# Kernel tuning notes

Measured on AMD Instinct MI355X. Metric: run time of the kernel, lower is better.

The kernel has to match this reference:

```python
import jax, jax.numpy as jnp
import numpy as np

B, T, SEQ = 8, 129, 128
H, N, NL, NE, V = 512, 64, 4, 128, 18

def _gelu(x):
    return jax.nn.gelu(x, approximate=False)

def _conv2d(x, w, b, stride):
    y = jax.lax.conv_general_dilated(x, w, (stride, stride), 'VALID',
                                     dimension_numbers=('NCHW', 'OIHW', 'NCHW'))
    return y + b[None, :, None, None]

def _layernorm(x, g, b, eps=1e-5):
    mu = jnp.mean(x, axis=-1, keepdims=True)
    var = jnp.mean(jnp.square(x - mu), axis=-1, keepdims=True)
    return (x - mu) * jax.lax.rsqrt(var + eps) * g + b

def _s4_kernel(log_dt, A_re, A_im, C_re, C_im, L):
    # Diagonal SSM (ZOH discretization, B=1): K[h,l] = 2*Re(sum_n Ceff * exp(dt*A)^l)
    dt = jnp.exp(log_dt)[:, None]                  # [H,1]
    A = A_re + 1j * A_im                            # [H,N] complex64
    dtA = (dt * A).astype(jnp.complex64)
    C = (C_re + 1j * C_im).astype(jnp.complex64)
    Ceff = C * (jnp.exp(dtA) - 1.0) / A             # [H,N]
    vand = jnp.exp(dtA[:, :, None] * jnp.arange(L, dtype=jnp.float32))  # [H,N,L]
    return 2.0 * jnp.einsum('hn,hnl->hl', Ceff, vand).real

def _fft_conv(u, K, D):
    # u: [B,H,L]  K: [H,L]  causal conv via zero-padded FFT
    L = u.shape[-1]
    n = 2 * L
    Uf = jnp.fft.rfft(u, n=n)
    Kf = jnp.fft.rfft(K, n=n)
    y = jnp.fft.irfft(Uf * Kf[None], n=n)[..., :L]
    return y + D[None, :, None] * u

def setup_inputs() -> dict:
    key = jax.random.key(0)
    ks = jax.random.split(key, 32)
    d = {}
    d['states'] = jax.random.uniform(ks[0], (B, T, 4, 84, 84), dtype=jnp.float32)
    d['actions'] = jax.random.randint(ks[1], (B, T), 0, V)
    d['rtgs'] = jax.random.uniform(ks[2], (B, T, 1), dtype=jnp.float32)
    s = 0.02
    d['enc_w1'] = jax.random.normal(ks[3], (32, 4, 8, 8)) * s
    d['enc_b1'] = jnp.zeros((32,))
    d['enc_w2'] = jax.random.normal(ks[4], (64, 32, 4, 4)) * s
    d['enc_b2'] = jnp.zeros((64,))
    d['enc_w3'] = jax.random.normal(ks[5], (64, 64, 3, 3)) * s
    d['enc_b3'] = jnp.zeros((64,))
    d['enc_lw'] = jax.random.normal(ks[6], (3136, NE)) * s
    d['enc_lb'] = jnp.zeros((NE,))
    d['ret_w'] = jax.random.normal(ks[7], (1, NE)) * s
    d['ret_b'] = jnp.zeros((NE,))
    d['act_emb'] = jax.random.normal(ks[8], (V, NE)) * s
    d['proj_w'] = jax.random.normal(ks[9], (3 * NE, H)) * s
    d['proj_b'] = jnp.zeros((H,))
    d['pre_w'] = jax.random.normal(ks[10], (H, H)) * s
    d['pre_b'] = jnp.zeros((H,))
    d['ln_g'] = jnp.ones((NL, H))
    d['ln_b'] = jnp.zeros((NL, H))
    lo, hi = np.log(1e-3), np.log(1e-1)
    d['log_dt'] = lo + jax.random.uniform(ks[11], (NL, H)) * (hi - lo)
    d['A_re'] = -0.5 * jnp.ones((NL, H, N))
    d['A_im'] = jnp.broadcast_to(np.pi * jnp.arange(N, dtype=jnp.float32), (NL, H, N)).copy()
    d['C_re'] = jax.random.normal(ks[12], (NL, H, N)) * (0.5 ** 0.5)
    d['C_im'] = jax.random.normal(ks[13], (NL, H, N)) * (0.5 ** 0.5)
    d['Dp'] = jax.random.normal(ks[14], (NL, H))
    d['aft_w'] = jax.random.normal(ks[15], (NL, H, H)) * s
    d['aft_b'] = jnp.zeros((NL, H))
    d['out_w'] = jax.random.normal(ks[16], (H, V)) * s
    return d

def reference(states, actions, rtgs, enc_w1, enc_b1, enc_w2, enc_b2, enc_w3, enc_b3,
              enc_lw, enc_lb, ret_w, ret_b, act_emb, proj_w, proj_b, pre_w, pre_b,
              ln_g, ln_b, log_dt, A_re, A_im, C_re, C_im, Dp, aft_w, aft_b, out_w):
    S = actions.shape[1] - 1  # del_r = 1
    # state encoder over B*S frames
    x = states[:, 1:].reshape(-1, 4, 84, 84)
    x = jax.nn.relu(_conv2d(x, enc_w1, enc_b1, 4))
    x = jax.nn.relu(_conv2d(x, enc_w2, enc_b2, 2))
    x = jax.nn.relu(_conv2d(x, enc_w3, enc_b3, 1))
    se = jnp.tanh(x.reshape(x.shape[0], -1) @ enc_lw + enc_lb)          # [B*S, NE]
    ae = jnp.tanh(act_emb[actions[:, :S].reshape(-1)])                   # [B*S, NE]
    re = jnp.tanh(rtgs[:, :S].reshape(-1, 1) @ ret_w + ret_b)            # [B*S, NE]
    u = jnp.concatenate([se, ae, re], axis=-1) @ proj_w + proj_b
    u = u.reshape(states.shape[0], S, H)
    y = _gelu(u) @ pre_w + pre_b                                          # beforeblock
    for i in range(NL):
        r = _layernorm(y, ln_g[i], ln_b[i])
        v = jnp.transpose(r, (0, 2, 1))                                   # [B,H,S]
        K = _s4_kernel(log_dt[i], A_re[i], A_im[i], C_re[i], C_im[i], S)
        c = _fft_conv(v, K, Dp[i])
        c = jnp.transpose(c, (0, 2, 1))                                   # [B,S,H]
        c = _gelu(_gelu(c) @ aft_w[i] + aft_b[i])
        y = c + y                                                          # s4_resnet
    logits = y @ out_w                                                     # [B,S,V]
    return logits
```

## Files before the change

kernel.cpp:

```cpp
#include <hip/hip_runtime.h>

#define Bq 8
#define Tq 129
#define Sq 128
#define Hq 512
#define Nq 64
#define NLq 4
#define NEq 128
#define Vq 18

typedef unsigned short u16;
typedef unsigned int u32;
typedef __attribute__((ext_vector_type(8))) short short8v;
typedef __attribute__((ext_vector_type(4))) float f32x4;

__device__ __forceinline__ float gelu_f(float x) {
  return 0.5f * x * (1.0f + erff(x * 0.70710678118654752f));
}

__device__ __forceinline__ u16 f2b(float x) {
  union { float f; unsigned int u; } v; v.f = x;
  unsigned int r = v.u + 0x7FFFu + ((v.u >> 16) & 1u);
  return (u16)(r >> 16);
}

__device__ __forceinline__ float b2f_lo(u32 u) {
  union { unsigned int u; float f; } v; v.u = u << 16; return v.f;
}
__device__ __forceinline__ float b2f_hi(u32 u) {
  union { unsigned int u; float f; } v; v.u = u & 0xffff0000u; return v.f;
}

__global__ __launch_bounds__(256) void wprep_k(const float* __restrict__ w1,
    const float* __restrict__ w2, const float* __restrict__ w3,
    u16* __restrict__ B1t, u16* __restrict__ B2t, u16* __restrict__ B3t) {
  int i = blockIdx.x * 256 + threadIdx.x;
  if (i < 8192) {
    int n = i >> 8, k = i & 255;
    int ic = k >> 6, ky = (k >> 3) & 7, kx = k & 7;
    B1t[i] = f2b(w1[((n * 4 + ic) * 8 + ky) * 8 + kx]);
  } else if (i < 8192 + 32768) {
    int j = i - 8192;
    int n = j >> 9, k = j & 511;
    int kyx = k >> 5, ic = k & 31, ky = kyx >> 2, kx = kyx & 3;
    B2t[j] = f2b(w2[((n * 32 + ic) * 4 + ky) * 4 + kx]);
  } else if (i < 8192 + 32768 + 36864) {
    int j = i - 40960;
    int n = j / 576, k = j - n * 576;
    int ic = k & 63, kyx = k >> 6, ky = kyx / 3, kx = kyx % 3;
    B3t[j] = f2b(w3[((n * 64 + ic) * 3 + ky) * 3 + kx]);
  }
}

__global__ __launch_bounds__(256) void wtrans_k(const float* __restrict__ enc_lw,
    const float* __restrict__ proj_w, const float* __restrict__ pre_w,
    const float* __restrict__ aft_w, const float* __restrict__ out_w,
    u16* __restrict__ Wt_enc, u16* __restrict__ Wt_proj, u16* __restrict__ Wt_pre,
    u16* __restrict__ Wt_aft, u16* __restrict__ Wt_out) {
  __shared__ u16 T[64][65];
  int bid = blockIdx.x;
  const float* src; u16* dst; int K, N, kt, nt, t;
  if (bid < 98)       { t = bid;       src = enc_lw; dst = Wt_enc;  K = 3136; N = 128; kt = t >> 1; nt = t & 1; }
  else if (bid < 146) { t = bid - 98;  src = proj_w; dst = Wt_proj; K = 384;  N = 512; kt = t >> 3; nt = t & 7; }
  else if (bid < 210) { t = bid - 146; src = pre_w;  dst = Wt_pre;  K = 512;  N = 512; kt = t >> 3; nt = t & 7; }
  else if (bid < 466) { t = bid - 210; int L = t >> 6; t &= 63;
                        src = aft_w + (size_t)L * 262144; dst = Wt_aft + (size_t)L * 262144;
                        K = 512; N = 512; kt = t >> 3; nt = t & 7; }
  else                { t = bid - 466; src = out_w;  dst = Wt_out;  K = 512;  N = 18;  kt = t;      nt = 0; }
  int k0 = kt * 64, n0 = nt * 64;
  #pragma unroll
  for (int it = 0; it < 16; it++) {
    int idx = it * 256 + threadIdx.x;
    int rr = idx >> 6, cc = idx & 63;
    float v = (n0 + cc < N) ? src[(size_t)(k0 + rr) * N + n0 + cc] : 0.f;
    T[cc][rr] = f2b(v);
  }
  __syncthreads();
  #pragma unroll
  for (int it = 0; it < 16; it++) {
    int idx = it * 256 + threadIdx.x;
    int rr = idx >> 6, cc = idx & 63;
    dst[(size_t)(n0 + rr) * K + k0 + cc] = T[rr][cc];
  }
}

template<bool AF32, int EPI>
__global__ __launch_bounds__(256) void mgemm(const void* __restrict__ Av,
    const u16* __restrict__ Wt, const float* __restrict__ bias,
    const float* __restrict__ res, void* __restrict__ Cv,
    int M, int K, int N, int ldc) {
  __shared__ u16 As[64][40];
  __shared__ u16 Bs[64][40];
  int tid = threadIdx.x;
  int bn = blockIdx.x * 64, bm = blockIdx.y * 64;
  int lane = tid & 63, w = tid >> 6;
  int q = lane >> 4, r = lane & 15;
  int wm = (w >> 1) * 32, wn = (w & 1) * 32;
  int am = tid >> 2, ak = (tid & 3) * 8;
  f32x4 acc[2][2] = {};
  for (int k0 = 0; k0 < K; k0 += 32) {
    if constexpr (AF32) {
      const float* A = (const float*)Av;
      const float* src = A + (size_t)(bm + am) * K + k0 + ak;
      float4 v0 = *(const float4*)src;
      float4 v1 = *(const float4*)(src + 4);
      ushort4 lo, hi;
      lo.x = f2b(v0.x); lo.y = f2b(v0.y); lo.z = f2b(v0.z); lo.w = f2b(v0.w);
      hi.x = f2b(v1.x); hi.y = f2b(v1.y); hi.z = f2b(v1.z); hi.w = f2b(v1.w);
      *(ushort4*)&As[am][ak] = lo;
      *(ushort4*)&As[am][ak + 4] = hi;
    } else {
      const u16* A = (const u16*)Av;
      *(short8v*)&As[am][ak] = *(const short8v*)(A + (size_t)(bm + am) * K + k0 + ak);
    }
    *(short8v*)&Bs[am][ak] = *(const short8v*)(Wt + (size_t)(bn + am) * K + k0 + ak);
    __syncthreads();
    short8v a0 = *(const short8v*)&As[wm + r][q * 8];
    short8v a1 = *(const short8v*)&As[wm + 16 + r][q * 8];
    short8v b0 = *(const short8v*)&Bs[wn + r][q * 8];
    short8v b1 = *(const short8v*)&Bs[wn + 16 + r][q * 8];
    acc[0][0] = __builtin_amdgcn_mfma_f32_16x16x32_bf16(a0, b0, acc[0][0], 0, 0, 0);
    acc[0][1] = __builtin_amdgcn_mfma_f32_16x16x32_bf16(a0, b1, acc[0][1], 0, 0, 0);
    acc[1][0] = __builtin_amdgcn_mfma_f32_16x16x32_bf16(a1, b0, acc[1][0], 0, 0, 0);
    acc[1][1] = __builtin_amdgcn_mfma_f32_16x16x32_bf16(a1, b1, acc[1][1], 0, 0, 0);
    __syncthreads();
  }
  #pragma unroll
  for (int ms = 0; ms < 2; ms++) {
    #pragma unroll
    for (int ns = 0; ns < 2; ns++) {
      #pragma unroll
      for (int reg = 0; reg < 4; reg++) {
        int m = bm + wm + ms * 16 + q * 4 + reg;
        int n = bn + wn + ns * 16 + r;
        if (n < N) {
          float v = acc[ms][ns][reg] + (bias ? bias[n] : 0.f);
          if (EPI == 0) ((float*)Cv)[(size_t)m * ldc + n] = v;
          if (EPI == 2) ((u16*)Cv)[(size_t)m * ldc + n] = f2b(gelu_f(v));
          if (EPI == 3) ((float*)Cv)[(size_t)m * ldc + n] = gelu_f(v) + res[(size_t)m * ldc + n];
        }
      }
    }
  }
}

__global__ __launch_bounds__(256) void enc_gemm(const u16* __restrict__ A,
    const u16* __restrict__ Wt, float* __restrict__ Cp) {
  __shared__ u16 As[64][40];
  __shared__ u16 Bs[64][40];
  int tid = threadIdx.x;
  int bn = blockIdx.x * 64, bm = blockIdx.y * 64, kc = blockIdx.z;
  int lane = tid & 63, w = tid >> 6;
  int q = lane >> 4, r = lane & 15;
  int wm = (w >> 1) * 32, wn = (w & 1) * 32;
  int am = tid >> 2, ak = (tid & 3) * 8;
  f32x4 acc[2][2] = {};
  int kend = kc * 448 + 448;
  for (int k0 = kc * 448; k0 < kend; k0 += 32) {
    *(short8v*)&As[am][ak] = *(const short8v*)(A + (size_t)(bm + am) * 3136 + k0 + ak);
    *(short8v*)&Bs[am][ak] = *(const short8v*)(Wt + (size_t)(bn + am) * 3136 + k0 + ak);
    __syncthreads();
    short8v a0 = *(const short8v*)&As[wm + r][q * 8];
    short8v a1 = *(const short8v*)&As[wm + 16 + r][q * 8];
    short8v b0 = *(const short8v*)&Bs[wn + r][q * 8];
    short8v b1 = *(const short8v*)&Bs[wn + 16 + r][q * 8];
    acc[0][0] = __builtin_amdgcn_mfma_f32_16x16x32_bf16(a0, b0, acc[0][0], 0, 0, 0);
    acc[0][1] = __builtin_amdgcn_mfma_f32_16x16x32_bf16(a0, b1, acc[0][1], 0, 0, 0);
    acc[1][0] = __builtin_amdgcn_mfma_f32_16x16x32_bf16(a1, b0, acc[1][0], 0, 0, 0);
    acc[1][1] = __builtin_amdgcn_mfma_f32_16x16x32_bf16(a1, b1, acc[1][1], 0, 0, 0);
    __syncthreads();
  }
  #pragma unroll
  for (int ms = 0; ms < 2; ms++)
    #pragma unroll
    for (int ns = 0; ns < 2; ns++)
      #pragma unroll
      for (int reg = 0; reg < 4; reg++) {
        int m = bm + wm + ms * 16 + q * 4 + reg;
        int n = bn + wn + ns * 16 + r;
        Cp[(size_t)(kc * 1024 + m) * 128 + n] = acc[ms][ns][reg];
      }
}

__global__ __launch_bounds__(256) void enc_red(const float* __restrict__ Cp,
    const float* __restrict__ bias, u16* __restrict__ uin) {
  int idx = blockIdx.x * 256 + threadIdx.x;
  int m = idx >> 7, n = idx & 127;
  float s = bias[n];
  #pragma unroll
  for (int kc = 0; kc < 7; kc++) s += Cp[(size_t)(kc * 1024 + m) * 128 + n];
  uin[(size_t)m * 384 + n] = f2b(tanhf(s));
}

__global__ __launch_bounds__(256) void conv1_mfma(const float* __restrict__ states,
    const u16* __restrict__ B1t, const float* __restrict__ bias, u16* __restrict__ out) {
  __shared__ u16 lds[28224];
  int fr = blockIdx.x;
  int b = fr >> 7, s = fr & 127;
  const float* in = states + (size_t)(b * Tq + s + 1) * 28224;
  int tid = threadIdx.x;
  #pragma unroll
  for (int it = 0; it < 28; it++) {
    int idx = tid + it * 256;
    if (idx < 7056) {
      float4 v = ((const float4*)in)[idx];
      ushort4 uv;
      uv.x = f2b(v.x); uv.y = f2b(v.y); uv.z = f2b(v.z); uv.w = f2b(v.w);
      *(ushort4*)&lds[idx * 4] = uv;
    }
  }
  int lane = tid & 63, w = tid >> 6;
  int q = lane >> 4, r = lane & 15;
  short8v bfr[2][8];
  #pragma unroll
  for (int nt = 0; nt < 2; nt++)
    #pragma unroll
    for (int ks = 0; ks < 8; ks++)
      bfr[nt][ks] = *(const short8v*)(B1t + (nt * 16 + r) * 256 + ks * 32 + q * 8);
  __syncthreads();
  for (int mt = w; mt < 25; mt += 4) {
    int m = mt * 16 + r;
    int oy = m / 20, ox = m % 20;
    f32x4 acc0 = {0.f, 0.f, 0.f, 0.f}, acc1 = {0.f, 0.f, 0.f, 0.f};
    #pragma unroll
    for (int ks = 0; ks < 8; ks++) {
      int k0 = ks * 32 + q * 8;
      int ic = k0 >> 6, ky = (k0 >> 3) & 7;
      int ai = ic * 7056 + (oy * 4 + ky) * 84 + ox * 4;
      ushort4 lo = *(const ushort4*)&lds[ai];
      ushort4 hi = *(const ushort4*)&lds[ai + 4];
      short8v av;
      av[0] = (short)lo.x; av[1] = (short)lo.y; av[2] = (short)lo.z; av[3] = (short)lo.w;
      av[4] = (short)hi.x; av[5] = (short)hi.y; av[6] = (short)hi.z; av[7] = (short)hi.w;
      acc0 = __builtin_amdgcn_mfma_f32_16x16x32_bf16(av, bfr[0][ks], acc0, 0, 0, 0);
      acc1 = __builtin_amdgcn_mfma_f32_16x16x32_bf16(av, bfr[1][ks], acc1, 0, 0, 0);
    }
    #pragma unroll
    for (int reg = 0; reg < 4; reg++) {
      int pos = mt * 16 + q * 4 + reg;
      out[(size_t)fr * 12800 + pos * 32 + r]      = f2b(fmaxf(acc0[reg] + bias[r], 0.f));
      out[(size_t)fr * 12800 + pos * 32 + 16 + r] = f2b(fmaxf(acc1[reg] + bias[16 + r], 0.f));
    }
  }
}

__global__ __launch_bounds__(256) void conv2_mfma(const u16* __restrict__ in_,
    const u16* __restrict__ B2t, const float* __restrict__ bias, u16* __restrict__ out) {
  __shared__ u16 lds[12800];
  int fr = blockIdx.x;
  int tid = threadIdx.x;
  const short8v* src = (const short8v*)(in_ + (size_t)fr * 12800);
  short8v* dst = (short8v*)lds;
  #pragma unroll
  for (int it = 0; it < 7; it++) {
    int idx = tid + it * 256;
    if (idx < 1600) dst[idx] = src[idx];
  }
  int lane = tid & 63, w = tid >> 6;
  int q = lane >> 4, r = lane & 15;
  int n = w * 16 + r;
  short8v bfr[16];
  #pragma unroll
  for (int ks = 0; ks < 16; ks++)
    bfr[ks] = *(const short8v*)(B2t + n * 512 + ks * 32 + q * 8);
  __syncthreads();
  float bn = bias[n];
  #pragma unroll
  for (int mt = 0; mt < 6; mt++) {
    int m = mt * 16 + r; if (m > 80) m = 80;
    int oy = m / 9, ox = m % 9;
    f32x4 acc = {0.f, 0.f, 0.f, 0.f};
    #pragma unroll
    for (int ks = 0; ks < 16; ks++) {
      int ky = ks >> 2, kx = ks & 3;
      int ai = ((oy * 2 + ky) * 20 + ox * 2 + kx) * 32 + q * 8;
      short8v av = *(const short8v*)&lds[ai];
      acc = __builtin_amdgcn_mfma_f32_16x16x32_bf16(av, bfr[ks], acc, 0, 0, 0);
    }
    #pragma unroll
    for (int reg = 0; reg < 4; reg++) {
      int pos = mt * 16 + q * 4 + reg;
      if (pos < 81)
        out[(size_t)fr * 5184 + pos * 64 + n] = f2b(fmaxf(acc[reg] + bn, 0.f));
    }
  }
}

__global__ __launch_bounds__(256) void conv3_mfma(const u16* __restrict__ in_,
    const u16* __restrict__ B3t, const float* __restrict__ bias, u16* __restrict__ out) {
  __shared__ u16 lds[5184];
  int fr = blockIdx.x;
  int tid = threadIdx.x;
  const short8v* src = (const short8v*)(in_ + (size_t)fr * 5184);
  short8v* dst = (short8v*)lds;
  #pragma unroll
  for (int it = 0; it < 3; it++) {
    int idx = tid + it * 256;
    if (idx < 648) dst[idx] = src[idx];
  }
  int lane = tid & 63, w = tid >> 6;
  int q = lane >> 4, r = lane & 15;
  int n = w * 16 + r;
  short8v bfr[18];
  #pragma unroll
  for (int ks = 0; ks < 18; ks++)
    bfr[ks] = *(const short8v*)(B3t + n * 576 + ks * 32 + q * 8);
  __syncthreads();
  float bn = bias[n];
  #pragma unroll
  for (int mt = 0; mt < 4; mt++) {
    int m = mt * 16 + r; if (m > 48) m = 48;
    int oy = m / 7, ox = m % 7;
    f32x4 acc = {0.f, 0.f, 0.f, 0.f};
    #pragma unroll
    for (int ks = 0; ks < 18; ks++) {
      int kyx = ks >> 1;
      int ky = kyx / 3, kx = kyx % 3;
      int ic0 = (ks & 1) * 32 + q * 8;
      int ai = ((oy + ky) * 9 + ox + kx) * 64 + ic0;
      short8v av = *(const short8v*)&lds[ai];
      acc = __builtin_amdgcn_mfma_f32_16x16x32_bf16(av, bfr[ks], acc, 0, 0, 0);
    }
    #pragma unroll
    for (int reg = 0; reg < 4; reg++) {
      int pos = mt * 16 + q * 4 + reg;
      if (pos < 49)
        out[(size_t)fr * 3136 + n * 49 + pos] = f2b(fmaxf(acc[reg] + bn, 0.f));
    }
  }
}

__global__ __launch_bounds__(256) void embed_k(const int* __restrict__ actions,
    const float* __restrict__ rtgs, const float* __restrict__ act_emb,
    const float* __restrict__ ret_w, const float* __restrict__ ret_b,
    u16* __restrict__ uin) {
  int f = blockIdx.x;
  int b = f >> 7, s = f & 127;
  int e = threadIdx.x;
  if (e < 128) {
    int a = actions[b * Tq + s];
    uin[(size_t)f * 384 + 128 + e] = f2b(tanhf(act_emb[a * NEq + e]));
  } else {
    int ee = e - 128;
    uin[(size_t)f * 384 + 256 + ee] =
        f2b(tanhf(fmaf(rtgs[b * Tq + s], ret_w[ee], ret_b[ee])));
  }
}

__global__ __launch_bounds__(64) void s4k_gen(const float* __restrict__ log_dt,
    const float* __restrict__ A_re, const float* __restrict__ A_im,
    const float* __restrict__ C_re, const float* __restrict__ C_im,
    u16* __restrict__ Ktb) {
  __shared__ float con[64][129];
  int lh = blockIdx.x;
  int n = threadIdx.x;
  float dt = expf(log_dt[lh]);
  float ar = A_re[(size_t)lh * Nq + n], ai = A_im[(size_t)lh * Nq + n];
  float al = dt * ar, be = dt * ai;
  float er = expf(al);
  float wr = er * cosf(be), wi = er * sinf(be);
  float zr = wr - 1.0f, zi = wi;
  float den = 1.0f / (ar * ar + ai * ai);
  float tr = (zr * ar + zi * ai) * den, ti = (zi * ar - zr * ai) * den;
  float Cr = C_re[(size_t)lh * Nq + n], Ci = C_im[(size_t)lh * Nq + n];
  float cr = Cr * tr - Ci * ti, ci = Cr * ti + Ci * tr;
  float curr = 1.0f, curi = 0.0f;
  for (int l = 0; l < Sq; l++) {
    con[n][l] = cr * curr - ci * curi;
    float nr = curr * wr - curi * wi;
    curi = curr * wi + curi * wr;
    curr = nr;
  }
  __syncthreads();
  int layer = lh >> 9, h = lh & 511;
  #pragma unroll
  for (int li = n; li < Sq; li += 64) {
    float s = 0.f;
    for (int j = 0; j < 64; j++) s += con[j][li];
    Ktb[((size_t)layer * Sq + li) * Hq + h] = f2b(2.0f * s);
  }
}

__global__ __launch_bounds__(256) void ln_k(const float* __restrict__ y,
    const float* __restrict__ g, const float* __restrict__ b, u16* __restrict__ r) {
  int row = blockIdx.x * 4 + (threadIdx.x >> 6);
  int lane = threadIdx.x & 63;
  const float* x = y + (size_t)row * Hq;
  float v[8], s = 0.f, s2 = 0.f;
  #pragma unroll
  for (int j = 0; j < 8; j++) {
    v[j] = x[lane + j * 64];
    s += v[j];
    s2 += v[j] * v[j];
  }
  #pragma unroll
  for (int o = 32; o >= 1; o >>= 1) {
    s += __shfl_xor(s, o);
    s2 += __shfl_xor(s2, o);
  }
  float mu = s * (1.f / Hq);
  float var = s2 * (1.f / Hq) - mu * mu;
  float inv = rsqrtf(var + 1e-5f);
  u16* out = r + (size_t)row * Hq;
  #pragma unroll
  for (int j = 0; j < 8; j++) {
    int h = lane + j * 64;
    out[h] = f2b((v[j] - mu) * inv * g[h] + b[h]);
  }
}

__global__ __launch_bounds__(256) void sconv_k(const u16* __restrict__ r,
    const u16* __restrict__ Kt, const float* __restrict__ D, u16* __restrict__ cact) {
  int s = blockIdx.x, b = blockIdx.y;
  int t = threadIdx.x;
  const u32* rb = (const u32*)(r + (size_t)b * Sq * Hq) + t;
  const u32* kp = (const u32*)Kt + t;
  float2 d = ((const float2*)D)[t];
  u32 rs = rb[(size_t)s * 256];
  float acc0 = d.x * b2f_lo(rs), acc1 = d.y * b2f_hi(rs);
  int j = 0;
  for (; j + 4 <= s + 1; j += 4) {
    u32 k0 = kp[(size_t)(j + 0) * 256];
    u32 k1 = kp[(size_t)(j + 1) * 256];
    u32 k2 = kp[(size_t)(j + 2) * 256];
    u32 k3 = kp[(size_t)(j + 3) * 256];
    u32 r0 = rb[(size_t)(s - j - 0) * 256];
    u32 r1 = rb[(size_t)(s - j - 1) * 256];
    u32 r2 = rb[(size_t)(s - j - 2) * 256];
    u32 r3 = rb[(size_t)(s - j - 3) * 256];
    acc0 = fmaf(b2f_lo(k0), b2f_lo(r0), acc0); acc1 = fmaf(b2f_hi(k0), b2f_hi(r0), acc1);
    acc0 = fmaf(b2f_lo(k1), b2f_lo(r1), acc0); acc1 = fmaf(b2f_hi(k1), b2f_hi(r1), acc1);
    acc0 = fmaf(b2f_lo(k2), b2f_lo(r2), acc0); acc1 = fmaf(b2f_hi(k2), b2f_hi(r2), acc1);
    acc0 = fmaf(b2f_lo(k3), b2f_lo(r3), acc0); acc1 = fmaf(b2f_hi(k3), b2f_hi(r3), acc1);
  }
  for (; j <= s; j++) {
    u32 kv = kp[(size_t)j * 256];
    u32 rv = rb[(size_t)(s - j) * 256];
    acc0 = fmaf(b2f_lo(kv), b2f_lo(rv), acc0);
    acc1 = fmaf(b2f_hi(kv), b2f_hi(rv), acc1);
  }
  u32 outv = (u32)f2b(gelu_f(acc0)) | ((u32)f2b(gelu_f(acc1)) << 16);
  ((u32*)(cact + ((size_t)b * Sq + s) * Hq))[t] = outv;
}

extern "C" void kernel_launch(void* const* d_in, const int* in_sizes, int n_in,
                              void* d_out, int out_size, void* d_ws, size_t ws_size,
                              hipStream_t stream) {
  const float* states  = (const float*)d_in[0];
  const int*   actions = (const int*)  d_in[1];
  const float* rtgs    = (const float*)d_in[2];
  const float* enc_w1  = (const float*)d_in[3];
  const float* enc_b1  = (const float*)d_in[4];
  const float* enc_w2  = (const float*)d_in[5];
  const float* enc_b2  = (const float*)d_in[6];
  const float* enc_w3  = (const float*)d_in[7];
  const float* enc_b3  = (const float*)d_in[8];
  const float* enc_lw  = (const float*)d_in[9];
  const float* enc_lb  = (const float*)d_in[10];
  const float* ret_w   = (const float*)d_in[11];
  const float* ret_b   = (const float*)d_in[12];
  const float* act_emb = (const float*)d_in[13];
  const float* proj_w  = (const float*)d_in[14];
  const float* proj_b  = (const float*)d_in[15];
  const float* pre_w   = (const float*)d_in[16];
  const float* pre_b   = (const float*)d_in[17];
  const float* ln_g    = (const float*)d_in[18];
  const float* ln_b    = (const float*)d_in[19];
  const float* log_dt  = (const float*)d_in[20];
  const float* A_re    = (const float*)d_in[21];
  const float* A_im    = (const float*)d_in[22];
  const float* C_re    = (const float*)d_in[23];
  const float* C_im    = (const float*)d_in[24];
  const float* Dp      = (const float*)d_in[25];
  const float* aft_w   = (const float*)d_in[26];
  const float* aft_b   = (const float*)d_in[27];
  const float* out_w   = (const float*)d_in[28];

  u16* Wt_enc  = (u16*)d_ws;
  u16* Wt_proj = Wt_enc + 401408;
  u16* Wt_pre  = Wt_proj + 196608;
  u16* Wt_aft  = Wt_pre + 262144;
  u16* Wt_out  = Wt_aft + 1048576;
  u16* B1t = Wt_out + 32768;
  u16* B2t = B1t + 8192;
  u16* B3t = B2t + 32768;
  u16* o1  = B3t + 36864;
  u16* o2  = o1 + 13107200;
  u16* x3b = o2 + 5308416;
  u16* uin = x3b + 3211264;
  u16* uact = uin + 393216;
  u16* cact = uact + 524288;
  u16* rb16 = cact + 524288;
  u16* Ktb  = rb16 + 524288;
  float* y  = (float*)(Ktb + 262144);
  float* Cp = y + 524288;

  wprep_k<<<304, 256, 0, stream>>>(enc_w1, enc_w2, enc_w3, B1t, B2t, B3t);
  wtrans_k<<<474, 256, 0, stream>>>(enc_lw, proj_w, pre_w, aft_w, out_w,
                                    Wt_enc, Wt_proj, Wt_pre, Wt_aft, Wt_out);
  conv1_mfma<<<1024, 256, 0, stream>>>(states, B1t, enc_b1, o1);
  conv2_mfma<<<1024, 256, 0, stream>>>(o1, B2t, enc_b2, o2);
  conv3_mfma<<<1024, 256, 0, stream>>>(o2, B3t, enc_b3, x3b);
  enc_gemm<<<dim3(2, 16, 7), 256, 0, stream>>>(x3b, Wt_enc, Cp);
  enc_red<<<512, 256, 0, stream>>>(Cp, enc_lb, uin);
  embed_k<<<1024, 256, 0, stream>>>(actions, rtgs, act_emb, ret_w, ret_b, uin);
  mgemm<false, 2><<<dim3(8, 16), 256, 0, stream>>>(uin, Wt_proj, proj_b, nullptr, uact,
                                                   1024, 384, 512, 512);
  mgemm<false, 0><<<dim3(8, 16), 256, 0, stream>>>(uact, Wt_pre, pre_b, nullptr, y,
                                                   1024, 512, 512, 512);
  s4k_gen<<<2048, 64, 0, stream>>>(log_dt, A_re, A_im, C_re, C_im, Ktb);

  for (int i = 0; i < NLq; i++) {
    ln_k<<<256, 256, 0, stream>>>(y, ln_g + i * Hq, ln_b + i * Hq, rb16);
    sconv_k<<<dim3(128, 8), 256, 0, stream>>>(rb16, Ktb + (size_t)i * Sq * Hq,
                                              Dp + i * Hq, cact);
    mgemm<false, 3><<<dim3(8, 16), 256, 0, stream>>>(cact, Wt_aft + (size_t)i * Hq * Hq,
                                                     aft_b + i * Hq, y, y,
                                                     1024, 512, 512, 512);
  }
  mgemm<true, 0><<<dim3(1, 16), 256, 0, stream>>>(y, Wt_out, nullptr, nullptr,
                                                  (float*)d_out, 1024, 512, Vq, Vq);
}
```

Measured before the change: 268.0 us.

## Merge prep kernels, fuse embed/reduce, tile causal conv in LDS, deepen GEMM K-stage

Merges the two weight-prep kernels into one launch and the encoder reduction with the embedding kernel. The layernorm apply step moves into a new LDS-tiled causal convolution that reuses kernel and input values across 8 outputs per thread, in place of strided global loads per output. The generic GEMM now stages 128 K elements per barrier pair, and conv1 runs with 512 threads. The aim is fewer launches, fewer barriers and less global traffic, at the cost of more LDS and registers and only 128 blocks for the conv kernel.

After: 225.8 us. 15.8% less time.

```diff
diff --git a/kernel.cpp b/kernel.cpp
--- a/kernel.cpp
+++ b/kernel.cpp
@@ -31,34 +31,36 @@
   union { unsigned int u; float f; } v; v.u = u & 0xffff0000u; return v.f;
 }
 
-__global__ __launch_bounds__(256) void wprep_k(const float* __restrict__ w1,
-    const float* __restrict__ w2, const float* __restrict__ w3,
+__global__ __launch_bounds__(256) void prep_k(
+    const float* __restrict__ enc_lw, const float* __restrict__ proj_w,
+    const float* __restrict__ pre_w, const float* __restrict__ aft_w,
+    const float* __restrict__ out_w,
+    const float* __restrict__ w1, const float* __restrict__ w2,
+    const float* __restrict__ w3,
+    u16* __restrict__ Wt_enc, u16* __restrict__ Wt_proj, u16* __restrict__ Wt_pre,
+    u16* __restrict__ Wt_aft, u16* __restrict__ Wt_out,
     u16* __restrict__ B1t, u16* __restrict__ B2t, u16* __restrict__ B3t) {
-  int i = blockIdx.x * 256 + threadIdx.x;
-  if (i < 8192) {
-    int n = i >> 8, k = i & 255;
-    int ic = k >> 6, ky = (k >> 3) & 7, kx = k & 7;
-    B1t[i] = f2b(w1[((n * 4 + ic) * 8 + ky) * 8 + kx]);
-  } else if (i < 8192 + 32768) {
-    int j = i - 8192;
-    int n = j >> 9, k = j & 511;
-    int kyx = k >> 5, ic = k & 31, ky = kyx >> 2, kx = kyx & 3;
-    B2t[j] = f2b(w2[((n * 32 + ic) * 4 + ky) * 4 + kx]);
-  } else if (i < 8192 + 32768 + 36864) {
-    int j = i - 40960;
-    int n = j / 576, k = j - n * 576;
-    int ic = k & 63, kyx = k >> 6, ky = kyx / 3, kx = kyx % 3;
-    B3t[j] = f2b(w3[((n * 64 + ic) * 3 + ky) * 3 + kx]);
-  }
-}
-
-__global__ __launch_bounds__(256) void wtrans_k(const float* __restrict__ enc_lw,
-    const float* __restrict__ proj_w, const float* __restrict__ pre_w,
-    const float* __restrict__ aft_w, const float* __restrict__ out_w,
-    u16* __restrict__ Wt_enc, u16* __restrict__ Wt_proj, u16* __restrict__ Wt_pre,
-    u16* __restrict__ Wt_aft, u16* __restrict__ Wt_out) {
   __shared__ u16 T[64][65];
   int bid = blockIdx.x;
+  if (bid >= 474) {
+    int i = (bid - 474) * 256 + threadIdx.x;
+    if (i < 8192) {
+      int n = i >> 8, k = i & 255;
+      int ic = k >> 6, ky = (k >> 3) & 7, kx = k & 7;
+      B1t[i] = f2b(w1[((n * 4 + ic) * 8 + ky) * 8 + kx]);
+    } else if (i < 8192 + 32768) {
+      int j = i - 8192;
+      int n = j >> 9, k = j & 511;
+      int kyx = k >> 5, ic = k & 31, ky = kyx >> 2, kx = kyx & 3;
+      B2t[j] = f2b(w2[((n * 32 + ic) * 4 + ky) * 4 + kx]);
+    } else if (i < 8192 + 32768 + 36864) {
+      int j = i - 40960;
+      int n = j / 576, k = j - n * 576;
+      int ic = k & 63, kyx = k >> 6, ky = kyx / 3, kx = kyx % 3;
+      B3t[j] = f2b(w3[((n * 64 + ic) * 3 + ky) * 3 + kx]);
+    }
+    return;
+  }
   const float* src; u16* dst; int K, N, kt, nt, t;
   if (bid < 98)       { t = bid;       src = enc_lw; dst = Wt_enc;  K = 3136; N = 128; kt = t >> 1; nt = t & 1; }
   else if (bid < 146) { t = bid - 98;  src = proj_w; dst = Wt_proj; K = 384;  N = 512; kt = t >> 3; nt = t & 7; }
@@ -89,40 +91,47 @@
     const u16* __restrict__ Wt, const float* __restrict__ bias,
     const float* __restrict__ res, void* __restrict__ Cv,
     int M, int K, int N, int ldc) {
-  __shared__ u16 As[64][40];
-  __shared__ u16 Bs[64][40];
+  __shared__ u16 As[4][64][40];
+  __shared__ u16 Bs[4][64][40];
   int tid = threadIdx.x;
   int bn = blockIdx.x * 64, bm = blockIdx.y * 64;
   int lane = tid & 63, w = tid >> 6;
   int q = lane >> 4, r = lane & 15;
   int wm = (w >> 1) * 32, wn = (w & 1) * 32;
-  int am = tid >> 2, ak = (tid & 3) * 8;
+  int am = tid >> 2, ak0 = (tid & 3) * 8;
   f32x4 acc[2][2] = {};
-  for (int k0 = 0; k0 < K; k0 += 32) {
-    if constexpr (AF32) {
-      const float* A = (const float*)Av;
-      const float* src = A + (size_t)(bm + am) * K + k0 + ak;
-      float4 v0 = *(const float4*)src;
-      float4 v1 = *(const float4*)(src + 4);
-      ushort4 lo, hi;
-      lo.x = f2b(v0.x); lo.y = f2b(v0.y); lo.z = f2b(v0.z); lo.w = f2b(v0.w);
-      hi.x = f2b(v1.x); hi.y = f2b(v1.y); hi.z = f2b(v1.z); hi.w = f2b(v1.w);
-      *(ushort4*)&As[am][ak] = lo;
-      *(ushort4*)&As[am][ak + 4] = hi;
-    } else {
-      const u16* A = (const u16*)Av;
-      *(short8v*)&As[am][ak] = *(const short8v*)(A + (size_t)(bm + am) * K + k0 + ak);
-    }
-    *(short8v*)&Bs[am][ak] = *(const short8v*)(Wt + (size_t)(bn + am) * K + k0 + ak);
+  for (int k0 = 0; k0 < K; k0 += 128) {
+    #pragma unroll
+    for (int st = 0; st < 4; st++) {
+      int kk = k0 + st * 32 + ak0;
+      if constexpr (AF32) {
+        const float* A = (const float*)Av;
+        const float* src = A + (size_t)(bm + am) * K + kk;
+        float4 v0 = *(const float4*)src;
+        float4 v1 = *(const float4*)(src + 4);
+        ushort4 lo, hi;
+        lo.x = f2b(v0.x); lo.y = f2b(v0.y); lo.z = f2b(v0.z); lo.w = f2b(v0.w);
+        hi.x = f2b(v1.x); hi.y = f2b(v1.y); hi.z = f2b(v1.z); hi.w = f2b(v1.w);
+        *(ushort4*)&As[st][am][ak0] = lo;
+        *(ushort4*)&As[st][am][ak0 + 4] = hi;
+      } else {
+        *(short8v*)&As[st][am][ak0] =
+            *(const short8v*)((const u16*)Av + (size_t)(bm + am) * K + kk);
+      }
+      *(short8v*)&Bs[st][am][ak0] = *(const short8v*)(Wt + (size_t)(bn + am) * K + kk);
+    }
     __syncthreads();
-    short8v a0 = *(const short8v*)&As[wm + r][q * 8];
-    short8v a1 = *(const short8v*)&As[wm + 16 + r][q * 8];
-    short8v b0 = *(const short8v*)&Bs[wn + r][q * 8];
-    short8v b1 = *(const short8v*)&Bs[wn + 16 + r][q * 8];
-    acc[0][0] = __builtin_amdgcn_mfma_f32_16x16x32_bf16(a0, b0, acc[0][0], 0, 0, 0);
-    acc[0][1] = __builtin_amdgcn_mfma_f32_16x16x32_bf16(a0, b1, acc[0][1], 0, 0, 0);
-    acc[1][0] = __builtin_amdgcn_mfma_f32_16x16x32_bf16(a1, b0, acc[1][0], 0, 0, 0);
-    acc[1][1] = __builtin_amdgcn_mfma_f32_16x16x32_bf16(a1, b1, acc[1][1], 0, 0, 0);
+    #pragma unroll
+    for (int st = 0; st < 4; st++) {
+      short8v a0 = *(const short8v*)&As[st][wm + r][q * 8];
+      short8v a1 = *(const short8v*)&As[st][wm + 16 + r][q * 8];
+      short8v b0 = *(const short8v*)&Bs[st][wn + r][q * 8];
+      short8v b1 = *(const short8v*)&Bs[st][wn + 16 + r][q * 8];
+      acc[0][0] = __builtin_amdgcn_mfma_f32_16x16x32_bf16(a0, b0, acc[0][0], 0, 0, 0);
+      acc[0][1] = __builtin_amdgcn_mfma_f32_16x16x32_bf16(a0, b1, acc[0][1], 0, 0, 0);
+      acc[1][0] = __builtin_amdgcn_mfma_f32_16x16x32_bf16(a1, b0, acc[1][0], 0, 0, 0);
+      acc[1][1] = __builtin_amdgcn_mfma_f32_16x16x32_bf16(a1, b1, acc[1][1], 0, 0, 0);
+    }
     __syncthreads();
   }
   #pragma unroll
@@ -182,17 +191,29 @@
       }
 }
 
-__global__ __launch_bounds__(256) void enc_red(const float* __restrict__ Cp,
-    const float* __restrict__ bias, u16* __restrict__ uin) {
-  int idx = blockIdx.x * 256 + threadIdx.x;
-  int m = idx >> 7, n = idx & 127;
-  float s = bias[n];
-  #pragma unroll
-  for (int kc = 0; kc < 7; kc++) s += Cp[(size_t)(kc * 1024 + m) * 128 + n];
-  uin[(size_t)m * 384 + n] = f2b(tanhf(s));
-}
-
-__global__ __launch_bounds__(256) void conv1_mfma(const float* __restrict__ states,
+__global__ __launch_bounds__(256) void embedred_k(const float* __restrict__ Cp,
+    const float* __restrict__ enc_lb, const int* __restrict__ actions,
+    const float* __restrict__ rtgs, const float* __restrict__ act_emb,
+    const float* __restrict__ ret_w, const float* __restrict__ ret_b,
+    u16* __restrict__ uin) {
+  int f = blockIdx.x;
+  int b = f >> 7, s = f & 127;
+  int e = threadIdx.x;
+  if (e < 128) {
+    float sum = enc_lb[e];
+    #pragma unroll
+    for (int kc = 0; kc < 7; kc++) sum += Cp[(size_t)(kc * 1024 + f) * 128 + e];
+    uin[(size_t)f * 384 + e] = f2b(tanhf(sum));
+    uin[(size_t)f * 384 + 256 + e] =
+        f2b(tanhf(fmaf(rtgs[b * Tq + s], ret_w[e], ret_b[e])));
+  } else {
+    int ee = e - 128;
+    int a = actions[b * Tq + s];
+    uin[(size_t)f * 384 + 128 + ee] = f2b(tanhf(act_emb[a * NEq + ee]));
+  }
+}
+
+__global__ __launch_bounds__(512) void conv1_mfma(const float* __restrict__ states,
     const u16* __restrict__ B1t, const float* __restrict__ bias, u16* __restrict__ out) {
   __shared__ u16 lds[28224];
   int fr = blockIdx.x;
@@ -200,8 +221,8 @@
   const float* in = states + (size_t)(b * Tq + s + 1) * 28224;
   int tid = threadIdx.x;
   #pragma unroll
-  for (int it = 0; it < 28; it++) {
-    int idx = tid + it * 256;
+  for (int it = 0; it < 14; it++) {
+    int idx = tid + it * 512;
     if (idx < 7056) {
       float4 v = ((const float4*)in)[idx];
       ushort4 uv;
@@ -218,7 +239,7 @@
     for (int ks = 0; ks < 8; ks++)
       bfr[nt][ks] = *(const short8v*)(B1t + (nt * 16 + r) * 256 + ks * 32 + q * 8);
   __syncthreads();
-  for (int mt = w; mt < 25; mt += 4) {
+  for (int mt = w; mt < 25; mt += 8) {
     int m = mt * 16 + r;
     int oy = m / 20, ox = m % 20;
     f32x4 acc0 = {0.f, 0.f, 0.f, 0.f}, acc1 = {0.f, 0.f, 0.f, 0.f};
@@ -327,23 +348,6 @@
       if (pos < 49)
         out[(size_t)fr * 3136 + n * 49 + pos] = f2b(fmaxf(acc[reg] + bn, 0.f));
     }
-  }
-}
-
-__global__ __launch_bounds__(256) void embed_k(const int* __restrict__ actions,
-    const float* __restrict__ rtgs, const float* __restrict__ act_emb,
-    const float* __restrict__ ret_w, const float* __restrict__ ret_b,
-    u16* __restrict__ uin) {
-  int f = blockIdx.x;
-  int b = f >> 7, s = f & 127;
-  int e = threadIdx.x;
-  if (e < 128) {
-    int a = actions[b * Tq + s];
-    uin[(size_t)f * 384 + 128 + e] = f2b(tanhf(act_emb[a * NEq + e]));
-  } else {
-    int ee = e - 128;
-    uin[(size_t)f * 384 + 256 + ee] =
-        f2b(tanhf(fmaf(rtgs[b * Tq + s], ret_w[ee], ret_b[ee])));
   }
 }
 
@@ -381,66 +385,100 @@
   }
 }
 
-__global__ __launch_bounds__(256) void ln_k(const float* __restrict__ y,
-    const float* __restrict__ g, const float* __restrict__ b, u16* __restrict__ r) {
+__global__ __launch_bounds__(256) void ln_stats(const float* __restrict__ y,
+    float2* __restrict__ stats) {
   int row = blockIdx.x * 4 + (threadIdx.x >> 6);
   int lane = threadIdx.x & 63;
   const float* x = y + (size_t)row * Hq;
-  float v[8], s = 0.f, s2 = 0.f;
+  float s = 0.f, s2 = 0.f;
   #pragma unroll
   for (int j = 0; j < 8; j++) {
-    v[j] = x[lane + j * 64];
-    s += v[j];
-    s2 += v[j] * v[j];
+    float v = x[lane + j * 64];
+    s += v; s2 += v * v;
   }
   #pragma unroll
   for (int o = 32; o >= 1; o >>= 1) {
     s += __shfl_xor(s, o);
     s2 += __shfl_xor(s2, o);
   }
-  float mu = s * (1.f / Hq);
-  float var = s2 * (1.f / Hq) - mu * mu;
-  float inv = rsqrtf(var + 1e-5f);
-  u16* out = r + (size_t)row * Hq;
-  #pragma unroll
-  for (int j = 0; j < 8; j++) {
-    int h = lane + j * 64;
-    out[h] = f2b((v[j] - mu) * inv * g[h] + b[h]);
-  }
-}
-
-__global__ __launch_bounds__(256) void sconv_k(const u16* __restrict__ r,
-    const u16* __restrict__ Kt, const float* __restrict__ D, u16* __restrict__ cact) {
-  int s = blockIdx.x, b = blockIdx.y;
+  if (lane == 0) {
+    float mu = s * (1.f / Hq);
+    float var = s2 * (1.f / Hq) - mu * mu;
+    stats[row] = make_float2(mu, rsqrtf(var + 1e-5f));
+  }
+}
+
+__global__ __launch_bounds__(256) void sconv_fused(const float* __restrict__ y,
+    const float2* __restrict__ stats, const float* __restrict__ g,
+    const float* __restrict__ bta, const u16* __restrict__ Kt,
+    const float* __restrict__ D, u16* __restrict__ cact) {
+  __shared__ u32 P[16][140];
+  __shared__ u32 KL[16][132];
+  int hc = blockIdx.x, b = blockIdx.y;
   int t = threadIdx.x;
-  const u32* rb = (const u32*)(r + (size_t)b * Sq * Hq) + t;
-  const u32* kp = (const u32*)Kt + t;
-  float2 d = ((const float2*)D)[t];
-  u32 rs = rb[(size_t)s * 256];
-  float acc0 = d.x * b2f_lo(rs), acc1 = d.y * b2f_hi(rs);
-  int j = 0;
-  for (; j + 4 <= s + 1; j += 4) {
-    u32 k0 = kp[(size_t)(j + 0) * 256];
-    u32 k1 = kp[(size_t)(j + 1) * 256];
-    u32 k2 = kp[(size_t)(j + 2) * 256];
-    u32 k3 = kp[(size_t)(j + 3) * 256];
-    u32 r0 = rb[(size_t)(s - j - 0) * 256];
-    u32 r1 = rb[(size_t)(s - j - 1) * 256];
-    u32 r2 = rb[(size_t)(s - j - 2) * 256];
-    u32 r3 = rb[(size_t)(s - j - 3) * 256];
-    acc0 = fmaf(b2f_lo(k0), b2f_lo(r0), acc0); acc1 = fmaf(b2f_hi(k0), b2f_hi(r0), acc1);
-    acc0 = fmaf(b2f_lo(k1), b2f_lo(r1), acc0); acc1 = fmaf(b2f_hi(k1), b2f_hi(r1), acc1);
-    acc0 = fmaf(b2f_lo(k2), b2f_lo(r2), acc0); acc1 = fmaf(b2f_hi(k2), b2f_hi(r2), acc1);
-    acc0 = fmaf(b2f_lo(k3), b2f_lo(r3), acc0); acc1 = fmaf(b2f_hi(k3), b2f_hi(r3), acc1);
-  }
-  for (; j <= s; j++) {
-    u32 kv = kp[(size_t)j * 256];
-    u32 rv = rb[(size_t)(s - j) * 256];
-    acc0 = fmaf(b2f_lo(kv), b2f_lo(rv), acc0);
-    acc1 = fmaf(b2f_hi(kv), b2f_hi(rv), acc1);
-  }
-  u32 outv = (u32)f2b(gelu_f(acc0)) | ((u32)f2b(gelu_f(acc1)) << 16);
-  ((u32*)(cact + ((size_t)b * Sq + s) * Hq))[t] = outv;
+  int h0 = hc * 32;
+  if (t < 16) {
+    #pragma unroll
+    for (int i = 0; i < 8; i++) P[t][i] = 0;
+  }
+  #pragma unroll
+  for (int it = 0; it < 8; it++) {
+    int idx = it * 256 + t;
+    int p = idx & 15, j = idx >> 4;
+    KL[p][j] = *(const u32*)(Kt + (size_t)j * Hq + h0 + 2 * p);
+  }
+  #pragma unroll
+  for (int it = 0; it < 8; it++) {
+    int idx = it * 256 + t;
+    int p = idx & 15, s = idx >> 4;
+    int row = b * Sq + s;
+    float2 v = *(const float2*)(y + (size_t)row * Hq + h0 + 2 * p);
+    float2 st = stats[row];
+    float2 gg = *(const float2*)(g + h0 + 2 * p);
+    float2 bb = *(const float2*)(bta + h0 + 2 * p);
+    float r0 = (v.x - st.x) * st.y * gg.x + bb.x;
+    float r1 = (v.y - st.x) * st.y * gg.y + bb.y;
+    P[p][8 + s] = (u32)f2b(r0) | ((u32)f2b(r1) << 16);
+  }
+  __syncthreads();
+  int p = t & 15, sg = t >> 4;
+  int s0 = sg * 8;
+  float acc0[8], acc1[8];
+  float2 d2 = *(const float2*)(D + h0 + 2 * p);
+  #pragma unroll
+  for (int k = 0; k < 8; k++) {
+    u32 rv = P[p][8 + s0 + k];
+    acc0[k] = d2.x * b2f_lo(rv);
+    acc1[k] = d2.y * b2f_hi(rv);
+  }
+  for (int jb = 0; jb <= sg; jb++) {
+    int base = (sg - jb) * 8;
+    u32 wv[16], kv[8];
+    *(uint4*)&wv[0]  = *(const uint4*)&P[p][base];
+    *(uint4*)&wv[4]  = *(const uint4*)&P[p][base + 4];
+    *(uint4*)&wv[8]  = *(const uint4*)&P[p][base + 8];
+    *(uint4*)&wv[12] = *(const uint4*)&P[p][base + 12];
+    *(uint4*)&kv[0]  = *(const uint4*)&KL[p][jb * 8];
+    *(uint4*)&kv[4]  = *(const uint4*)&KL[p][jb * 8 + 4];
+    float wlo[16], whi[16], klo[8], khi[8];
+    #pragma unroll
+    for (int i = 0; i < 16; i++) { wlo[i] = b2f_lo(wv[i]); whi[i] = b2f_hi(wv[i]); }
+    #pragma unroll
+    for (int i = 0; i < 8; i++) { klo[i] = b2f_lo(kv[i]); khi[i] = b2f_hi(kv[i]); }
+    #pragma unroll
+    for (int jo = 0; jo < 8; jo++)
+      #pragma unroll
+      for (int k = 0; k < 8; k++) {
+        acc0[k] = fmaf(klo[jo], wlo[8 + k - jo], acc0[k]);
+        acc1[k] = fmaf(khi[jo], whi[8 + k - jo], acc1[k]);
+      }
+  }
+  #pragma unroll
+  for (int k = 0; k < 8; k++) {
+    int s = s0 + k;
+    u32 outv = (u32)f2b(gelu_f(acc0[k])) | ((u32)f2b(gelu_f(acc1[k])) << 16);
+    *(u32*)(cact + ((size_t)(b * Sq + s)) * Hq + h0 + 2 * p) = outv;
+  }
 }
 
 extern "C" void kernel_launch(void* const* d_in, const int* in_sizes, int n_in,
@@ -490,20 +528,21 @@
   u16* uin = x3b + 3211264;
   u16* uact = uin + 393216;
   u16* cact = uact + 524288;
-  u16* rb16 = cact + 524288;
-  u16* Ktb  = rb16 + 524288;
-  float* y  = (float*)(Ktb + 262144);
-  float* Cp = y + 524288;
-
-  wprep_k<<<304, 256, 0, stream>>>(enc_w1, enc_w2, enc_w3, B1t, B2t, B3t);
-  wtrans_k<<<474, 256, 0, stream>>>(enc_lw, proj_w, pre_w, aft_w, out_w,
-                                    Wt_enc, Wt_proj, Wt_pre, Wt_aft, Wt_out);
-  conv1_mfma<<<1024, 256, 0, stream>>>(states, B1t, enc_b1, o1);
+  u16* Ktb  = cact + 524288;
+  float* y    = (float*)(Ktb + 262144);
+  float* Cp   = y + 524288;
+  float2* stats = (float2*)(Cp + 917504);
+
+  prep_k<<<778, 256, 0, stream>>>(enc_lw, proj_w, pre_w, aft_w, out_w,
+                                  enc_w1, enc_w2, enc_w3,
+                                  Wt_enc, Wt_proj, Wt_pre, Wt_aft, Wt_out,
+                                  B1t, B2t, B3t);
+  conv1_mfma<<<1024, 512, 0, stream>>>(states, B1t, enc_b1, o1);
   conv2_mfma<<<1024, 256, 0, stream>>>(o1, B2t, enc_b2, o2);
   conv3_mfma<<<1024, 256, 0, stream>>>(o2, B3t, enc_b3, x3b);
   enc_gemm<<<dim3(2, 16, 7), 256, 0, stream>>>(x3b, Wt_enc, Cp);
-  enc_red<<<512, 256, 0, stream>>>(Cp, enc_lb, uin);
-  embed_k<<<1024, 256, 0, stream>>>(actions, rtgs, act_emb, ret_w, ret_b, uin);
+  embedred_k<<<1024, 256, 0, stream>>>(Cp, enc_lb, actions, rtgs, act_emb,
+                                       ret_w, ret_b, uin);
   mgemm<false, 2><<<dim3(8, 16), 256, 0, stream>>>(uin, Wt_proj, proj_b, nullptr, uact,
                                                    1024, 384, 512, 512);
   mgemm<false, 0><<<dim3(8, 16), 256, 0, stream>>>(uact, Wt_pre, pre_b, nullptr, y,
@@ -511,9 +550,11 @@
   s4k_gen<<<2048, 64, 0, stream>>>(log_dt, A_re, A_im, C_re, C_im, Ktb);
 
   for (int i = 0; i < NLq; i++) {
-    ln_k<<<256, 256, 0, stream>>>(y, ln_g + i * Hq, ln_b + i * Hq, rb16);
-    sconv_k<<<dim3(128, 8), 256, 0, stream>>>(rb16, Ktb + (size_t)i * Sq * Hq,
-                                              Dp + i * Hq, cact);
+    ln_stats<<<256, 256, 0, stream>>>(y, stats);
+    sconv_fused<<<dim3(16, 8), 256, 0, stream>>>(y, stats, ln_g + i * Hq,
+                                                 ln_b + i * Hq,
+                                                 Ktb + (size_t)i * Sq * Hq,
+                                                 Dp + i * Hq, cact);
     mgemm<false, 3><<<dim3(8, 16), 256, 0, stream>>>(cact, Wt_aft + (size_t)i * Hq * Hq,
                                                      aft_b + i * Hq, y, y,
                                                      1024, 512, 512, 512);
```
